# Performance work log

Hardware: AMD Instinct MI355X
Metric: run time of the kernel (lower is better)

## Reference

```python
import jax, jax.numpy as jnp
import numpy as np

T, D, E, F, K = 2048, 1024, 16, 512, 2  # tokens, hidden, experts, expert d_ff, top_k
NORM_TOPK = True


def setup_inputs() -> dict:
    key = jax.random.key(0)
    k0, k1, k2, k3 = jax.random.split(key, 4)
    hidden_states = jax.random.normal(k0, (T, D), jnp.float32)
    w_gate = jax.random.normal(k1, (E, D), jnp.float32) * (D ** -0.5)      # router Linear(D, E), no bias
    w13 = jax.random.normal(k2, (E, 2 * F, D), jnp.float32) * (D ** -0.5)  # fused gate+up proj per expert
    w2 = jax.random.normal(k3, (E, D, F), jnp.float32) * (F ** -0.5)       # down proj per expert
    return {"hidden_states": hidden_states, "w_gate": w_gate, "w13": w13, "w2": w2}


def reference(hidden_states, w_gate, w13, w2):
    # Router: softmax (fp32) -> top-k -> optional renorm
    logits = hidden_states @ w_gate.T                                   # [T, E]
    probs = jax.nn.softmax(logits.astype(jnp.float32), axis=-1)
    weights, selected = jax.lax.top_k(probs, K)                          # [T, K]
    if NORM_TOPK:
        weights = weights / jnp.sum(weights, axis=-1, keepdims=True)
    weights = weights.astype(hidden_states.dtype)

    # Sparse combine matrix: combine[t, e] = routing weight iff expert e selected for token t
    combine = jnp.zeros((T, E), hidden_states.dtype)
    combine = combine.at[jnp.arange(T)[:, None], selected].add(weights)

    # Expert FFN (computed for all experts, zeroed by combine; faithful math)
    h = jnp.einsum('td,efd->tef', hidden_states, w13)                    # [T, E, 2F]
    gate, up = jnp.split(h, 2, axis=-1)
    act = jax.nn.silu(gate) * up                                         # SiluAndMul, [T, E, F]
    y = jnp.einsum('tef,edf->ted', act, w2)                              # [T, E, D]
    return jnp.einsum('ted,te->td', y, combine)                          # [T, D]
```

## Files before the change

### kernel.cpp

```cpp
#include <hip/hip_runtime.h>
#include <hip/hip_bf16.h>
#include <math.h>

#define T_TOK 2048
#define DIM   1024
#define NEXP  16
#define FDIM  512
#define TOPK  2

#define BM 128
#define BN 64
#define BK 32

typedef float f32x4 __attribute__((ext_vector_type(4)));
typedef short s16x8 __attribute__((ext_vector_type(8)));

static __device__ __forceinline__ ushort f2bf(float f) {
  union { float f; unsigned u; } v; v.f = f;
  unsigned u = v.u;
  unsigned r = u + 0x7fffu + ((u >> 16) & 1u);
  return (ushort)(r >> 16);
}
static __device__ __forceinline__ float bf2f(ushort h) {
  union { unsigned u; float f; } v; v.u = ((unsigned)h) << 16; return v.f;
}
static __device__ __forceinline__ void split2(float f, ushort& h, ushort& l) {
  ushort hb = f2bf(f);
  h = hb;
  l = f2bf(f - bf2f(hb));
}

union u4s8 { uint4 u; s16x8 s; };
static __device__ __forceinline__ s16x8 as8(uint4 v) { u4s8 c; c.u = v; return c.s; }

static __device__ __forceinline__ void conv8(float4 f0, float4 f1, s16x8& h, s16x8& l) {
  float fs[8] = {f0.x, f0.y, f0.z, f0.w, f1.x, f1.y, f1.z, f1.w};
  uint hp[4], lp[4];
#pragma unroll
  for (int j = 0; j < 4; ++j) {
    ushort ha, la, hb, lb;
    split2(fs[2 * j], ha, la);
    split2(fs[2 * j + 1], hb, lb);
    hp[j] = (uint)ha | ((uint)hb << 16);
    lp[j] = (uint)la | ((uint)lb << 16);
  }
  uint4 hu = make_uint4(hp[0], hp[1], hp[2], hp[3]);
  uint4 lu = make_uint4(lp[0], lp[1], lp[2], lp[3]);
  h = as8(hu); l = as8(lu);
}

static __device__ __forceinline__ void gload16(const void* g, const void* l) {
  __builtin_amdgcn_global_load_lds(
      (const __attribute__((address_space(1))) void*)g,
      (__attribute__((address_space(3))) void*)l, 16, 0, 0);
}

static __device__ __forceinline__ int inv_swz64(int p) {
  int q6 = ((p >> 6) ^ (p >> 8)) & 1;
  int q5 = ((p >> 5) ^ (p >> 7)) & 1;
  int q4 = ((p >> 4) ^ (p >> 6) ^ (p >> 8)) & 1;
  return (p & ~0x70) | (q4 << 4) | (q5 << 5) | (q6 << 6);
}

__global__ __launch_bounds__(64) void router_k(const float* __restrict__ x,
                                               const float* __restrict__ wg,
                                               int* __restrict__ sel,
                                               float* __restrict__ wt,
                                               int* __restrict__ cnt) {
  int t = blockIdx.x;
  int lane = threadIdx.x;
  const float* xr = x + (size_t)t * DIM;
  float acc[NEXP];
#pragma unroll
  for (int e = 0; e < NEXP; ++e) acc[e] = 0.f;
  for (int d0 = 0; d0 < DIM; d0 += 64) {
    float xv = xr[d0 + lane];
#pragma unroll
    for (int e = 0; e < NEXP; ++e) acc[e] += xv * wg[e * DIM + d0 + lane];
  }
#pragma unroll
  for (int e = 0; e < NEXP; ++e) {
    float v = acc[e];
    v += __shfl_xor(v, 32); v += __shfl_xor(v, 16); v += __shfl_xor(v, 8);
    v += __shfl_xor(v, 4);  v += __shfl_xor(v, 2);  v += __shfl_xor(v, 1);
    acc[e] = v;
  }
  if (lane == 0) {
    float b1 = -1e30f, b2 = -1e30f; int i1 = 0, i2 = 0;
#pragma unroll
    for (int e = 0; e < NEXP; ++e) {
      float v = acc[e];
      if (v > b1) { b2 = b1; i2 = i1; b1 = v; i1 = e; }
      else if (v > b2) { b2 = v; i2 = e; }
    }
    float r = expf(b2 - b1);
    float w2v = r / (1.f + r);
    float w1v = 1.f - w2v;
    sel[t * 2 + 0] = i1; sel[t * 2 + 1] = i2;
    wt[t * 2 + 0] = w1v; wt[t * 2 + 1] = w2v;
    atomicAdd(&cnt[i1], 1);
    atomicAdd(&cnt[i2], 1);
  }
}

__global__ __launch_bounds__(256) void xsplit_k(const float* __restrict__ x,
                                                ushort* __restrict__ xhi,
                                                ushort* __restrict__ xlo) {
  int idx = (blockIdx.x * 256 + threadIdx.x) * 4;
  float4 v = *(const float4*)(x + idx);
  ushort h0,h1,h2,h3,l0,l1,l2,l3;
  split2(v.x, h0, l0); split2(v.y, h1, l1);
  split2(v.z, h2, l2); split2(v.w, h3, l3);
  *(ushort4*)(xhi + idx) = make_ushort4(h0, h1, h2, h3);
  *(ushort4*)(xlo + idx) = make_ushort4(l0, l1, l2, l3);
}

__global__ void offsets_k(const int* __restrict__ cnt, int* __restrict__ off) {
  if (threadIdx.x == 0 && blockIdx.x == 0) {
    int s = 0;
#pragma unroll
    for (int e = 0; e < NEXP; ++e) { off[e] = s; s += cnt[e]; }
    off[NEXP] = s;
  }
}

__global__ __launch_bounds__(256) void fill_k(const int* __restrict__ sel,
                                              const float* __restrict__ wt,
                                              const int* __restrict__ off,
                                              int* __restrict__ cnt2,
                                              int* __restrict__ rowtok,
                                              float* __restrict__ rowwt) {
  int i = blockIdx.x * 256 + threadIdx.x;
  if (i >= T_TOK * TOPK) return;
  int e = sel[i];
  int pos = off[e] + atomicAdd(&cnt2[e], 1);
  rowtok[pos] = i >> 1;
  rowwt[pos] = wt[i];
}


#define MOE_STAGE(AhB, AlB, BfB, KB)                                         \
  do {                                                                       \
    gload16(gA00 + (KB), (const char*)(AhB) + ldsA0);                        \
    gload16(gA10 + (KB), (const char*)(AhB) + ldsA1);                        \
    gload16(gA01 + (KB), (const char*)(AlB) + ldsA0);                        \
    gload16(gA11 + (KB), (const char*)(AlB) + ldsA1);                        \
    gload16(gB0 + (KB), (const char*)(BfB) + ldsB0);                         \
    gload16(gB1 + (KB), (const char*)(BfB) + ldsB1);                         \
  } while (0)

#define MOE_COMPUTE(AhB, AlB, BfB)                                           \
  do {                                                                       \
    float4 br00 = *(const float4*)((const char*)(BfB) + boff00);             \
    float4 br01 = *(const float4*)((const char*)(BfB) + boff01);             \
    float4 br10 = *(const float4*)((const char*)(BfB) + boff10);             \
    float4 br11 = *(const float4*)((const char*)(BfB) + boff11);             \
    s16x8 bh0, bl0, bh1, bl1;                                                \
    conv8(br00, br01, bh0, bl0);                                             \
    conv8(br10, br11, bh1, bl1);                                             \
    _Pragma("unroll")                                                        \
    for (int fm = 0; fm < 4; ++fm) {                                         \
      s16x8 ah = *(const s16x8*)((const char*)(AhB) + aoff[fm]);             \
      s16x8 al = *(const s16x8*)((const char*)(AlB) + aoff[fm]);             \
      acc[fm][0] = __builtin_amdgcn_mfma_f32_16x16x32_bf16(ah, bh0, acc[fm][0], 0, 0, 0); \
      acc[fm][0] = __builtin_amdgcn_mfma_f32_16x16x32_bf16(ah, bl0, acc[fm][0], 0, 0, 0); \
      acc[fm][0] = __builtin_amdgcn_mfma_f32_16x16x32_bf16(al, bh0, acc[fm][0], 0, 0, 0); \
      acc[fm][1] = __builtin_amdgcn_mfma_f32_16x16x32_bf16(ah, bh1, acc[fm][1], 0, 0, 0); \
      acc[fm][1] = __builtin_amdgcn_mfma_f32_16x16x32_bf16(ah, bl1, acc[fm][1], 0, 0, 0); \
      acc[fm][1] = __builtin_amdgcn_mfma_f32_16x16x32_bf16(al, bh1, acc[fm][1], 0, 0, 0); \
    }                                                                        \
  } while (0)

#define MOE_SYNC()                                                           \
  do {                                                                       \
    asm volatile("s_waitcnt vmcnt(0) lgkmcnt(0)" ::: "memory");              \
    __builtin_amdgcn_s_barrier();                                            \
    __builtin_amdgcn_sched_barrier(0);                                       \
  } while (0)

#define MOE_READ_OFFSETS()                                                   \
  int wm = (w & 1) * 64, wn = (w >> 1) * 32;                                 \
  int lr = lane & 15, lk = lane >> 4;                                        \
  int aoff[4];                                                               \
  _Pragma("unroll")                                                          \
  for (int fm = 0; fm < 4; ++fm) {                                           \
    int row = wm + fm * 16 + lr;                                             \
    aoff[fm] = (row * 64 + lk * 16) ^ ((row & 7) << 4);                      \
  }                                                                          \
  int brow0 = wn + 0 * 16 + lr, brow1 = wn + 1 * 16 + lr;                    \
  int boff00 = brow0 * 128 + ((lk * 32) ^ ((brow0 & 7) << 4));               \
  int boff01 = brow0 * 128 + (((lk * 32) + 16) ^ ((brow0 & 7) << 4));        \
  int boff10 = brow1 * 128 + ((lk * 32) ^ ((brow1 & 7) << 4));               \
  int boff11 = brow1 * 128 + (((lk * 32) + 16) ^ ((brow1 & 7) << 4));

__global__ __launch_bounds__(256, 4) void gemm1_k(const ushort* __restrict__ xhi,
                                                  const ushort* __restrict__ xlo,
                                                  const float* __restrict__ w13,
                                                  const int* __restrict__ off,
                                                  const int* __restrict__ rowtok,
                                                  float* __restrict__ H) {
  const int NS = DIM / BK;
  int e = blockIdx.z;
  int rbeg = off[e];
  int rows = off[e + 1] - rbeg;
  int m0 = blockIdx.y * BM;
  if (m0 >= rows) return;
  int n0 = blockIdx.x * BN;

  __shared__ ushort Ah[2][BM * BK];
  __shared__ ushort Al[2][BM * BK];
  __shared__ float  Bf[2][BN * BK];

  int tid = threadIdx.x;
  int lane = tid & 63;
  int w = tid >> 6;

  int ldsA0 = w * 2048, ldsA1 = w * 2048 + 1024;
  int ldsB0 = ldsA0, ldsB1 = ldsA1;
  const ushort *gA00, *gA10, *gA01, *gA11;
  {
    int p0 = ldsA0 + lane * 16, p1 = ldsA1 + lane * 16;
    int q0 = inv_swz64(p0), q1 = inv_swz64(p1);
    int r0 = m0 + (q0 >> 6); r0 = r0 < rows ? r0 : rows - 1;
    int r1 = m0 + (q1 >> 6); r1 = r1 < rows ? r1 : rows - 1;
    size_t b0 = (size_t)rowtok[rbeg + r0] * DIM + ((q0 & 63) >> 1);
    size_t b1 = (size_t)rowtok[rbeg + r1] * DIM + ((q1 & 63) >> 1);
    gA00 = xhi + b0; gA10 = xhi + b1;
    gA01 = xlo + b0; gA11 = xlo + b1;
  }
  const float *gB0, *gB1;
  {
    int p0 = ldsB0 + lane * 16, p1 = ldsB1 + lane * 16;
    int r0 = p0 >> 7, r1 = p1 >> 7;
    int c0 = ((p0 & 127) ^ ((r0 & 7) << 4)) >> 2;
    int c1 = ((p1 & 127) ^ ((r1 & 7) << 4)) >> 2;
    gB0 = w13 + ((size_t)e * (2 * FDIM) + (n0 + r0)) * DIM + c0;
    gB1 = w13 + ((size_t)e * (2 * FDIM) + (n0 + r1)) * DIM + c1;
  }

  MOE_READ_OFFSETS()

  f32x4 acc[4][2];
#pragma unroll
  for (int a = 0; a < 4; ++a)
#pragma unroll
    for (int b = 0; b < 2; ++b) acc[a][b] = {0.f, 0.f, 0.f, 0.f};

  MOE_STAGE(Ah[0], Al[0], Bf[0], 0);
  MOE_SYNC();

#pragma unroll 2
  for (int ks = 0; ks < NS; ++ks) {
    int cur = ks & 1;
    if (ks + 1 < NS) {
      if (cur == 0) MOE_STAGE(Ah[1], Al[1], Bf[1], (ks + 1) * BK);
      else          MOE_STAGE(Ah[0], Al[0], Bf[0], (ks + 1) * BK);
    }
    if (cur == 0) MOE_COMPUTE(Ah[0], Al[0], Bf[0]);
    else          MOE_COMPUTE(Ah[1], Al[1], Bf[1]);
    MOE_SYNC();
  }

#pragma unroll
  for (int fm = 0; fm < 4; ++fm) {
    int rloc = wm + fm * 16 + lk * 4;
#pragma unroll
    for (int j = 0; j < 4; ++j) {
      int row = rloc + j;
      if (m0 + row < rows) {
        size_t gr = (size_t)(rbeg + m0 + row) * (2 * FDIM);
#pragma unroll
        for (int fn = 0; fn < 2; ++fn)
          H[gr + n0 + wn + fn * 16 + lr] = acc[fm][fn][j];
      }
    }
  }
}

__global__ __launch_bounds__(256) void act_k(const float* __restrict__ H,
                                             ushort* __restrict__ ahi,
                                             ushort* __restrict__ alo) {
  int idx = (blockIdx.x * 256 + threadIdx.x) * 4;
  int r = idx >> 9;
  int f = idx & 511;
  const float* hrow = H + (size_t)r * (2 * FDIM);
  float4 g = *(const float4*)(hrow + f);
  float4 u = *(const float4*)(hrow + FDIM + f);
  float a0 = g.x / (1.f + expf(-g.x)) * u.x;
  float a1 = g.y / (1.f + expf(-g.y)) * u.y;
  float a2 = g.z / (1.f + expf(-g.z)) * u.z;
  float a3 = g.w / (1.f + expf(-g.w)) * u.w;
  ushort h0,h1,h2,h3,l0,l1,l2,l3;
  split2(a0, h0, l0); split2(a1, h1, l1);
  split2(a2, h2, l2); split2(a3, h3, l3);
  *(ushort4*)(ahi + (size_t)r * FDIM + f) = make_ushort4(h0, h1, h2, h3);
  *(ushort4*)(alo + (size_t)r * FDIM + f) = make_ushort4(l0, l1, l2, l3);
}

__global__ __launch_bounds__(256, 4) void gemm2_k(const ushort* __restrict__ ahi,
                                                  const ushort* __restrict__ alo,
                                                  const float* __restrict__ w2,
                                                  const int* __restrict__ off,
                                                  const int* __restrict__ rowtok,
                                                  const float* __restrict__ rowwt,
                                                  float* __restrict__ out) {
  const int NS = FDIM / BK;
  int e = blockIdx.z;
  int rbeg = off[e];
  int rows = off[e + 1] - rbeg;
  int m0 = blockIdx.y * BM;
  if (m0 >= rows) return;
  int n0 = blockIdx.x * BN;

  __shared__ ushort Ah[2][BM * BK];
  __shared__ ushort Al[2][BM * BK];
  __shared__ float  Bf[2][BN * BK];

  int tid = threadIdx.x;
  int lane = tid & 63;
  int w = tid >> 6;

  int ldsA0 = w * 2048, ldsA1 = w * 2048 + 1024;
  int ldsB0 = ldsA0, ldsB1 = ldsA1;
  const ushort *gA00, *gA10, *gA01, *gA11;
  {
    int p0 = ldsA0 + lane * 16, p1 = ldsA1 + lane * 16;
    int q0 = inv_swz64(p0), q1 = inv_swz64(p1);
    int r0 = m0 + (q0 >> 6); r0 = r0 < rows ? r0 : rows - 1;
    int r1 = m0 + (q1 >> 6); r1 = r1 < rows ? r1 : rows - 1;
    size_t b0 = (size_t)(rbeg + r0) * FDIM + ((q0 & 63) >> 1);
    size_t b1 = (size_t)(rbeg + r1) * FDIM + ((q1 & 63) >> 1);
    gA00 = ahi + b0; gA10 = ahi + b1;
    gA01 = alo + b0; gA11 = alo + b1;
  }
  const float *gB0, *gB1;
  {
    int p0 = ldsB0 + lane * 16, p1 = ldsB1 + lane * 16;
    int r0 = p0 >> 7, r1 = p1 >> 7;
    int c0 = ((p0 & 127) ^ ((r0 & 7) << 4)) >> 2;
    int c1 = ((p1 & 127) ^ ((r1 & 7) << 4)) >> 2;
    gB0 = w2 + ((size_t)e * DIM + (n0 + r0)) * FDIM + c0;
    gB1 = w2 + ((size_t)e * DIM + (n0 + r1)) * FDIM + c1;
  }

  MOE_READ_OFFSETS()

  f32x4 acc[4][2];
#pragma unroll
  for (int a = 0; a < 4; ++a)
#pragma unroll
    for (int b = 0; b < 2; ++b) acc[a][b] = {0.f, 0.f, 0.f, 0.f};

  MOE_STAGE(Ah[0], Al[0], Bf[0], 0);
  MOE_SYNC();

#pragma unroll 2
  for (int ks = 0; ks < NS; ++ks) {
    int cur = ks & 1;
    if (ks + 1 < NS) {
      if (cur == 0) MOE_STAGE(Ah[1], Al[1], Bf[1], (ks + 1) * BK);
      else          MOE_STAGE(Ah[0], Al[0], Bf[0], (ks + 1) * BK);
    }
    if (cur == 0) MOE_COMPUTE(Ah[0], Al[0], Bf[0]);
    else          MOE_COMPUTE(Ah[1], Al[1], Bf[1]);
    MOE_SYNC();
  }

#pragma unroll
  for (int fm = 0; fm < 4; ++fm) {
    int rloc = wm + fm * 16 + lk * 4;
#pragma unroll
    for (int j = 0; j < 4; ++j) {
      int row = rloc + j;
      if (m0 + row < rows) {
        int idx = rbeg + m0 + row;
        int tok = rowtok[idx];
        float wgt = rowwt[idx];
        float* orow = out + (size_t)tok * DIM + n0;
#pragma unroll
        for (int fn = 0; fn < 2; ++fn)
          atomicAdd(orow + wn + fn * 16 + lr, wgt * acc[fm][fn][j]);
      }
    }
  }
}

extern "C" void kernel_launch(void* const* d_in, const int* in_sizes, int n_in,
                              void* d_out, int out_size, void* d_ws, size_t ws_size,
                              hipStream_t stream) {
  const float* x   = (const float*)d_in[0];
  const float* wg  = (const float*)d_in[1];
  const float* w13 = (const float*)d_in[2];
  const float* w2  = (const float*)d_in[3];
  float* out = (float*)d_out;

  char* ws = (char*)d_ws;
  int*   cnt    = (int*)(ws + 0);
  int*   cnt2   = (int*)(ws + 64);
  int*   off    = (int*)(ws + 128);
  int*   sel    = (int*)(ws + 1024);
  float* wt     = (float*)(ws + 1024 + 16384);
  int*   rowtok = (int*)(ws + 1024 + 32768);
  float* rowwt  = (float*)(ws + 1024 + 49152);
  size_t o = 128 * 1024;
  ushort* xhi = (ushort*)(ws + o); o += (size_t)T_TOK * DIM * 2;
  ushort* xlo = (ushort*)(ws + o); o += (size_t)T_TOK * DIM * 2;
  float*  H   = (float*)(ws + o);  o += (size_t)T_TOK * TOPK * 2 * FDIM * 4;
  ushort* ahi = (ushort*)(ws + o); o += (size_t)T_TOK * TOPK * FDIM * 2;
  ushort* alo = (ushort*)(ws + o); o += (size_t)T_TOK * TOPK * FDIM * 2;

  hipMemsetAsync(ws, 0, 256, stream);
  hipMemsetAsync(d_out, 0, (size_t)out_size * sizeof(float), stream);

  router_k<<<T_TOK, 64, 0, stream>>>(x, wg, sel, wt, cnt);
  xsplit_k<<<(T_TOK * DIM) / 1024, 256, 0, stream>>>(x, xhi, xlo);
  offsets_k<<<1, 64, 0, stream>>>(cnt, off);
  fill_k<<<(T_TOK * TOPK + 255) / 256, 256, 0, stream>>>(sel, wt, off, cnt2, rowtok, rowwt);

  dim3 g1(2 * FDIM / BN, T_TOK / BM, NEXP);
  gemm1_k<<<g1, 256, 0, stream>>>(xhi, xlo, w13, off, rowtok, H);

  act_k<<<(T_TOK * TOPK * FDIM) / 1024, 256, 0, stream>>>(H, ahi, alo);

  dim3 g2(DIM / BN, T_TOK / BM, NEXP);
  gemm2_k<<<g2, 256, 0, stream>>>(ahi, alo, w2, off, rowtok, rowwt, out);
}
```

Before: 295.2 us.

## Deepen GEMM B-prefetch pipeline and aggregate routing atomics in shared memory

Both expert GEMMs move to a pipeline that prefetches the fp32 weight tile two K-steps ahead, using a third B buffer in shared memory, and waits only on partial vmcnt so loads stay in flight across barriers. Launch bounds drop from 4 to 2 blocks per SM to make room for the larger LDS footprint and registers. Routing counts now come from a separate histogram kernel that aggregates per block in shared memory, and fill_k assigns positions with block-local ranks plus one global atomic per expert. The aim is to hide global load latency in the GEMMs and cut contended global atomics, at the cost of lower occupancy and one extra launch.

New measurement: 292.8 us. Within noise of the previous version (-0.8%).

```diff
diff --git a/kernel.cpp b/kernel.cpp
--- a/kernel.cpp
+++ b/kernel.cpp
@@ -65,8 +65,7 @@
 __global__ __launch_bounds__(64) void router_k(const float* __restrict__ x,
                                                const float* __restrict__ wg,
                                                int* __restrict__ sel,
-                                               float* __restrict__ wt,
-                                               int* __restrict__ cnt) {
+                                               float* __restrict__ wt) {
   int t = blockIdx.x;
   int lane = threadIdx.x;
   const float* xr = x + (size_t)t * DIM;
@@ -98,8 +97,6 @@
     float w1v = 1.f - w2v;
     sel[t * 2 + 0] = i1; sel[t * 2 + 1] = i2;
     wt[t * 2 + 0] = w1v; wt[t * 2 + 1] = w2v;
-    atomicAdd(&cnt[i1], 1);
-    atomicAdd(&cnt[i2], 1);
   }
 }
 
@@ -115,6 +112,18 @@
   *(ushort4*)(xlo + idx) = make_ushort4(l0, l1, l2, l3);
 }
 
+__global__ __launch_bounds__(256) void hist_k(const int* __restrict__ sel,
+                                              int* __restrict__ cnt) {
+  __shared__ int h[NEXP];
+  int tid = threadIdx.x;
+  if (tid < NEXP) h[tid] = 0;
+  __syncthreads();
+  int i = blockIdx.x * 256 + tid;
+  atomicAdd(&h[sel[i]], 1);
+  __syncthreads();
+  if (tid < NEXP) atomicAdd(&cnt[tid], h[tid]);
+}
+
 __global__ void offsets_k(const int* __restrict__ cnt, int* __restrict__ off) {
   if (threadIdx.x == 0 && blockIdx.x == 0) {
     int s = 0;
@@ -130,21 +139,32 @@
                                               int* __restrict__ cnt2,
                                               int* __restrict__ rowtok,
                                               float* __restrict__ rowwt) {
-  int i = blockIdx.x * 256 + threadIdx.x;
-  if (i >= T_TOK * TOPK) return;
+  __shared__ int h[NEXP];
+  __shared__ int base[NEXP];
+  int tid = threadIdx.x;
+  if (tid < NEXP) h[tid] = 0;
+  __syncthreads();
+  int i = blockIdx.x * 256 + tid;
   int e = sel[i];
-  int pos = off[e] + atomicAdd(&cnt2[e], 1);
+  int lrank = atomicAdd(&h[e], 1);
+  __syncthreads();
+  if (tid < NEXP) base[tid] = atomicAdd(&cnt2[tid], h[tid]);
+  __syncthreads();
+  int pos = off[e] + base[e] + lrank;
   rowtok[pos] = i >> 1;
   rowwt[pos] = wt[i];
 }
 
-
-#define MOE_STAGE(AhB, AlB, BfB, KB)                                         \
+#define MOE_STAGE_A(AhB, AlB, KB)                                            \
   do {                                                                       \
     gload16(gA00 + (KB), (const char*)(AhB) + ldsA0);                        \
     gload16(gA10 + (KB), (const char*)(AhB) + ldsA1);                        \
     gload16(gA01 + (KB), (const char*)(AlB) + ldsA0);                        \
     gload16(gA11 + (KB), (const char*)(AlB) + ldsA1);                        \
+  } while (0)
+
+#define MOE_STAGE_B(BfB, KB)                                                 \
+  do {                                                                       \
     gload16(gB0 + (KB), (const char*)(BfB) + ldsB0);                         \
     gload16(gB1 + (KB), (const char*)(BfB) + ldsB1);                         \
   } while (0)
@@ -171,11 +191,32 @@
     }                                                                        \
   } while (0)
 
-#define MOE_SYNC()                                                           \
+#define MOE_BAR()                                                            \
+  do { __builtin_amdgcn_s_barrier(); __builtin_amdgcn_sched_barrier(0); } while (0)
+
+#define MOE_PIPE_LOOP(NSv)                                                   \
   do {                                                                       \
+    MOE_STAGE_A(ahc, alc, 0);                                                \
+    MOE_STAGE_B(bfc, 0);                                                     \
+    MOE_STAGE_B(bf1, BK);                                                    \
+    asm volatile("s_waitcnt vmcnt(2)" ::: "memory");                         \
+    MOE_BAR();                                                               \
+    _Pragma("unroll 1")                                                      \
+    for (int ks = 0; ks < (NSv) - 2; ++ks) {                                 \
+      MOE_STAGE_A(ahn, aln, (ks + 1) * BK);                                  \
+      MOE_STAGE_B(bfn, (ks + 2) * BK);                                       \
+      MOE_COMPUTE(ahc, alc, bfc);                                            \
+      asm volatile("s_waitcnt vmcnt(2) lgkmcnt(0)" ::: "memory");            \
+      MOE_BAR();                                                             \
+      { ushort* t = ahc; ahc = ahn; ahn = t; }                               \
+      { ushort* t = alc; alc = aln; aln = t; }                               \
+      { float* t = bfc; bfc = bf1; bf1 = bfn; bfn = t; }                     \
+    }                                                                        \
+    MOE_STAGE_A(ahn, aln, ((NSv) - 1) * BK);                                 \
+    MOE_COMPUTE(ahc, alc, bfc);                                              \
     asm volatile("s_waitcnt vmcnt(0) lgkmcnt(0)" ::: "memory");              \
-    __builtin_amdgcn_s_barrier();                                            \
-    __builtin_amdgcn_sched_barrier(0);                                       \
+    MOE_BAR();                                                               \
+    MOE_COMPUTE(ahn, aln, bf1);                                              \
   } while (0)
 
 #define MOE_READ_OFFSETS()                                                   \
@@ -193,7 +234,7 @@
   int boff10 = brow1 * 128 + ((lk * 32) ^ ((brow1 & 7) << 4));               \
   int boff11 = brow1 * 128 + (((lk * 32) + 16) ^ ((brow1 & 7) << 4));
 
-__global__ __launch_bounds__(256, 4) void gemm1_k(const ushort* __restrict__ xhi,
+__global__ __launch_bounds__(256, 2) void gemm1_k(const ushort* __restrict__ xhi,
                                                   const ushort* __restrict__ xlo,
                                                   const float* __restrict__ w13,
                                                   const int* __restrict__ off,
@@ -209,7 +250,7 @@
 
   __shared__ ushort Ah[2][BM * BK];
   __shared__ ushort Al[2][BM * BK];
-  __shared__ float  Bf[2][BN * BK];
+  __shared__ float  Bf[3][BN * BK];
 
   int tid = threadIdx.x;
   int lane = tid & 63;
@@ -246,20 +287,11 @@
 #pragma unroll
     for (int b = 0; b < 2; ++b) acc[a][b] = {0.f, 0.f, 0.f, 0.f};
 
-  MOE_STAGE(Ah[0], Al[0], Bf[0], 0);
-  MOE_SYNC();
-
-#pragma unroll 2
-  for (int ks = 0; ks < NS; ++ks) {
-    int cur = ks & 1;
-    if (ks + 1 < NS) {
-      if (cur == 0) MOE_STAGE(Ah[1], Al[1], Bf[1], (ks + 1) * BK);
-      else          MOE_STAGE(Ah[0], Al[0], Bf[0], (ks + 1) * BK);
-    }
-    if (cur == 0) MOE_COMPUTE(Ah[0], Al[0], Bf[0]);
-    else          MOE_COMPUTE(Ah[1], Al[1], Bf[1]);
-    MOE_SYNC();
-  }
+  ushort *ahc = Ah[0], *ahn = Ah[1];
+  ushort *alc = Al[0], *aln = Al[1];
+  float  *bfc = Bf[0], *bf1 = Bf[1], *bfn = Bf[2];
+
+  MOE_PIPE_LOOP(NS);
 
 #pragma unroll
   for (int fm = 0; fm < 4; ++fm) {
@@ -297,7 +329,7 @@
   *(ushort4*)(alo + (size_t)r * FDIM + f) = make_ushort4(l0, l1, l2, l3);
 }
 
-__global__ __launch_bounds__(256, 4) void gemm2_k(const ushort* __restrict__ ahi,
+__global__ __launch_bounds__(256, 2) void gemm2_k(const ushort* __restrict__ ahi,
                                                   const ushort* __restrict__ alo,
                                                   const float* __restrict__ w2,
                                                   const int* __restrict__ off,
@@ -314,7 +346,7 @@
 
   __shared__ ushort Ah[2][BM * BK];
   __shared__ ushort Al[2][BM * BK];
-  __shared__ float  Bf[2][BN * BK];
+  __shared__ float  Bf[3][BN * BK];
 
   int tid = threadIdx.x;
   int lane = tid & 63;
@@ -351,20 +383,11 @@
 #pragma unroll
     for (int b = 0; b < 2; ++b) acc[a][b] = {0.f, 0.f, 0.f, 0.f};
 
-  MOE_STAGE(Ah[0], Al[0], Bf[0], 0);
-  MOE_SYNC();
-
-#pragma unroll 2
-  for (int ks = 0; ks < NS; ++ks) {
-    int cur = ks & 1;
-    if (ks + 1 < NS) {
-      if (cur == 0) MOE_STAGE(Ah[1], Al[1], Bf[1], (ks + 1) * BK);
-      else          MOE_STAGE(Ah[0], Al[0], Bf[0], (ks + 1) * BK);
-    }
-    if (cur == 0) MOE_COMPUTE(Ah[0], Al[0], Bf[0]);
-    else          MOE_COMPUTE(Ah[1], Al[1], Bf[1]);
-    MOE_SYNC();
-  }
+  ushort *ahc = Ah[0], *ahn = Ah[1];
+  ushort *alc = Al[0], *aln = Al[1];
+  float  *bfc = Bf[0], *bf1 = Bf[1], *bfn = Bf[2];
+
+  MOE_PIPE_LOOP(NS);
 
 #pragma unroll
   for (int fm = 0; fm < 4; ++fm) {
@@ -412,10 +435,11 @@
   hipMemsetAsync(ws, 0, 256, stream);
   hipMemsetAsync(d_out, 0, (size_t)out_size * sizeof(float), stream);
 
-  router_k<<<T_TOK, 64, 0, stream>>>(x, wg, sel, wt, cnt);
+  router_k<<<T_TOK, 64, 0, stream>>>(x, wg, sel, wt);
   xsplit_k<<<(T_TOK * DIM) / 1024, 256, 0, stream>>>(x, xhi, xlo);
+  hist_k<<<(T_TOK * TOPK) / 256, 256, 0, stream>>>(sel, cnt);
   offsets_k<<<1, 64, 0, stream>>>(cnt, off);
-  fill_k<<<(T_TOK * TOPK + 255) / 256, 256, 0, stream>>>(sel, wt, off, cnt2, rowtok, rowwt);
+  fill_k<<<(T_TOK * TOPK) / 256, 256, 0, stream>>>(sel, wt, off, cnt2, rowtok, rowwt);
 
   dim3 g1(2 * FDIM / BN, T_TOK / BM, NEXP);
   gemm1_k<<<g1, 256, 0, stream>>>(xhi, xlo, w13, off, rowtok, H);
```
